# Kernel optimization log

Measured on AMD Instinct MI355X. Metric: run time of the kernel, lower is better.

## Reference

```python
import jax, jax.numpy as jnp
import numpy as np

N_NODES = 100000
N_EDGES = 3200000
IN_C, HID_C, OUT_C = 64, 64, 32


def setup_inputs() -> dict:
    key = jax.random.key(0)
    ks = jax.random.split(key, 8)
    x = jax.random.normal(ks[0], (N_NODES, IN_C), dtype=jnp.float32)
    edge_index = jax.random.randint(ks[1], (2, N_EDGES), 0, N_NODES, dtype=jnp.int64)
    s1 = 1.0 / np.sqrt(IN_C)
    s2 = 1.0 / np.sqrt(HID_C)
    W1l = jax.random.uniform(ks[2], (IN_C, HID_C), jnp.float32, -s1, s1)
    b1l = jnp.zeros((HID_C,), jnp.float32)
    W1r = jax.random.uniform(ks[3], (IN_C, HID_C), jnp.float32, -s1, s1)
    W2l = jax.random.uniform(ks[4], (HID_C, OUT_C), jnp.float32, -s2, s2)
    b2l = jnp.zeros((OUT_C,), jnp.float32)
    W2r = jax.random.uniform(ks[5], (HID_C, OUT_C), jnp.float32, -s2, s2)
    return {"x": x, "edge_index": edge_index, "W1l": W1l, "b1l": b1l,
            "W1r": W1r, "W2l": W2l, "b2l": b2l, "W2r": W2r}


def _sage_conv(x, src, dst, Wl, bl, Wr):
    # mean-aggregate source features onto destination nodes
    msg = x[src]                                              # [E, d] gather
    summed = jax.ops.segment_sum(msg, dst, num_segments=N_NODES)
    deg = jax.ops.segment_sum(jnp.ones((src.shape[0],), x.dtype), dst,
                              num_segments=N_NODES)
    agg = summed / jnp.maximum(deg, 1.0)[:, None]             # [N, d]
    return agg @ Wl + bl + x @ Wr                             # lin_l(agg)+lin_r(x)


def reference(x, edge_index, W1l, b1l, W1r, W2l, b2l, W2r):
    src, dst = edge_index[0], edge_index[1]
    h = jax.nn.relu(_sage_conv(x, src, dst, W1l, b1l, W1r))
    # dropout is identity in eval mode
    return _sage_conv(h, src, dst, W2l, b2l, W2r)
```

## Files before the change

### kernel.cpp

```cpp
#include <hip/hip_runtime.h>
#include <hip/hip_bf16.h>

#define N_NODES 100000
#define N_EDGES 3200000
#define NBKT 391
#define BKT_CAP 10240
#define NOCT (N_NODES / 8)

typedef __hip_bfloat16 bf16;
typedef unsigned int uint;
typedef __attribute__((ext_vector_type(8))) short bf16x8;
typedef __attribute__((ext_vector_type(4))) float f32x4;

__device__ __forceinline__ float b2f(bf16 v) { return __bfloat162float(v); }

__device__ __forceinline__ float bits2f(unsigned short w) {
    union { unsigned short u; bf16 b; } c;
    c.u = w;
    return __bfloat162float(c.b);
}
__device__ __forceinline__ unsigned short f2bits(float f) {
    return (unsigned short)(__float_as_uint(f) >> 16);
}
__device__ __forceinline__ unsigned short f2bf_bits(float f) {
    bf16 b = __float2bfloat16(f);
    unsigned short u;
    __builtin_memcpy(&u, &b, 2);
    return u;
}
__device__ __forceinline__ float lo16f(uint w) { return __uint_as_float(w << 16); }
__device__ __forceinline__ float hi16f(uint w) { return __uint_as_float(w & 0xffff0000u); }

__device__ __forceinline__ int get_idx(const void* ei, long long pos, int is64) {
    if (is64) return (int)((const long long*)ei)[pos];
    return ((const int*)ei)[pos];
}
__device__ __forceinline__ float get_f(const void* p, long long pos, int isbf) {
    if (isbf) return b2f(((const bf16*)p)[pos]);
    return ((const float*)p)[pos];
}

__global__ void detect_kernel(const void* __restrict__ x,
                              const void* __restrict__ ei,
                              int* __restrict__ flags) {
    int lane = threadIdx.x;
    const unsigned short* xw = (const unsigned short*)x;
    float v = bits2f(xw[2 * lane]);
    bool plaus = (v == v) && fabsf(v) > 1e-3f && fabsf(v) < 1e2f;
    unsigned long long m1 = __ballot(plaus);
    const int* iw = (const int*)ei;
    bool z = (iw[2 * lane + 1] == 0);
    unsigned long long m2 = __ballot(z);
    if (lane == 0) {
        flags[0] = (__popcll(m1) >= 32) ? 1 : 0;
        flags[1] = (__popcll(m2) == 64) ? 1 : 0;
    }
}

__global__ __launch_bounds__(256) void transpose_kernel(
    const void* __restrict__ x, uint4* __restrict__ xt,
    const int* __restrict__ flags) {
    if (!flags[0]) return;
    int i = blockIdx.x * 256 + threadIdx.x;
    if (i >= N_NODES * 4) return;
    int node = i >> 2, cz = i & 3;
    const uint4* x4 = (const uint4*)x;
    uint4 a = x4[(long long)node * 8 + cz * 2];
    uint4 b = x4[(long long)node * 8 + cz * 2 + 1];
    long long o = (long long)cz * (N_NODES * 2) + (long long)node * 2;
    xt[o] = a;
    xt[o + 1] = b;
}

__global__ __launch_bounds__(256) void scatterA_kernel(
    const void* __restrict__ ei, int* __restrict__ bucket_cursor,
    uint* __restrict__ bucket_data, const int* __restrict__ flags) {
    __shared__ int lhist[NBKT];
    __shared__ int lbase[NBKT];
    int is64 = flags[1];
    int t = threadIdx.x;
    int chunk0 = blockIdx.x * 8192;
    int dreg[32];

    for (int i = t; i < NBKT; i += 256) lhist[i] = 0;
    __syncthreads();
#pragma unroll
    for (int j = 0; j < 32; j++) {
        int e = chunk0 + j * 256 + t;
        int d = -1;
        if (e < N_EDGES) {
            d = get_idx(ei, (long long)N_EDGES + e, is64);
            atomicAdd(&lhist[d >> 8], 1);
        }
        dreg[j] = d;
    }
    __syncthreads();
    for (int i = t; i < NBKT; i += 256) {
        int c = lhist[i];
        lbase[i] = c ? atomicAdd(&bucket_cursor[i], c) : 0;
        lhist[i] = 0;
    }
    __syncthreads();
#pragma unroll
    for (int j = 0; j < 32; j++) {
        int e = chunk0 + j * 256 + t;
        int d = dreg[j];
        if (d >= 0) {
            int s = get_idx(ei, e, is64);
            int b = d >> 8;
            int o = lbase[b] + atomicAdd(&lhist[b], 1);
            if (o < BKT_CAP)
                bucket_data[(long long)b * BKT_CAP + o] = ((uint)(d & 255) << 17) | (uint)s;
        }
    }
}

__global__ void scanBuckets_kernel(const int* __restrict__ cnt,
                                   int* __restrict__ base) {
    __shared__ int buf[512];
    int t = threadIdx.x;
    int v = (t < NBKT) ? cnt[t] : 0;
    buf[t] = v;
    __syncthreads();
    for (int off = 1; off < 512; off <<= 1) {
        int add = (t >= off) ? buf[t - off] : 0;
        __syncthreads();
        buf[t] += add;
        __syncthreads();
    }
    if (t < NBKT) base[t] = buf[t] - v;
}

__global__ __launch_bounds__(256) void csrB_kernel(
    const int* __restrict__ bucket_cnt, const int* __restrict__ bucket_base,
    const uint* __restrict__ bucket_data, int* __restrict__ csr_src,
    int* __restrict__ row_start) {
    __shared__ int lh[256];
    __shared__ int buf[256];
    int b = blockIdx.x;
    int t = threadIdx.x;
    int cnt = bucket_cnt[b];
    if (cnt > BKT_CAP) cnt = BKT_CAP;
    int base = bucket_base[b];
    const uint* bd = bucket_data + (long long)b * BKT_CAP;

    lh[t] = 0;
    __syncthreads();
    for (int i = t; i < cnt; i += 256) atomicAdd(&lh[bd[i] >> 17], 1);
    __syncthreads();
    int v = lh[t];
    buf[t] = v;
    __syncthreads();
    for (int off = 1; off < 256; off <<= 1) {
        int add = (t >= off) ? buf[t - off] : 0;
        __syncthreads();
        buf[t] += add;
        __syncthreads();
    }
    int excl = buf[t] - v;
    int g = (b << 8) + t;
    if (g < N_NODES) row_start[g] = base + excl;
    lh[t] = excl;
    __syncthreads();
    for (int i = t; i < cnt; i += 256) {
        uint e = bd[i];
        int o = atomicAdd(&lh[e >> 17], 1);
        csr_src[base + o] = (int)(e & 0x1FFFFu);
    }
    if (b == 0 && t == 0) row_start[N_NODES] = N_EDGES;
}

#define ACCF4(acc, v, v2)                                                        \
    acc[0] += __uint_as_float((v).x) + __uint_as_float((v2).x);                   \
    acc[1] += __uint_as_float((v).y) + __uint_as_float((v2).y);                   \
    acc[2] += __uint_as_float((v).z) + __uint_as_float((v2).z);                   \
    acc[3] += __uint_as_float((v).w) + __uint_as_float((v2).w);

__device__ __forceinline__ void slice_gather8(
    const uint* __restrict__ su, const int* __restrict__ row_start,
    const int* __restrict__ csr_src, int nb0, int g8, int c8, int lane,
    float& a0, float& a1, int& dg_out) {
    int rl = (lane <= 8) ? row_start[nb0 + lane] : 0;
    int sg = __shfl(rl, g8 >> 3, 64);
    int eg = __shfl(rl, (g8 >> 3) + 1, 64);
    int dg = eg - sg;
    int maxd = dg;
    maxd = max(maxd, __shfl_xor(maxd, 8, 64));
    maxd = max(maxd, __shfl_xor(maxd, 16, 64));
    maxd = max(maxd, __shfl_xor(maxd, 32, 64));

    float s0f = 0.0f, s1f = 0.0f;
    for (int base = 0; base < maxd; base += 8) {
        int pf = sg + base + c8;
        int sreg = (pf < eg) ? __builtin_nontemporal_load(csr_src + pf) : 0;
        int ss[8];
#pragma unroll
        for (int u = 0; u < 8; u++) ss[u] = __shfl(sreg, g8 + u, 64);
        uint wv[8];
#pragma unroll
        for (int u = 0; u < 8; u++)
            wv[u] = (base + u < dg) ? su[(ss[u] << 3) + c8] : 0u;
#pragma unroll
        for (int u = 0; u < 8; u++) {
            s0f += lo16f(wv[u]);
            s1f += hi16f(wv[u]);
        }
    }
    a0 = s0f;
    a1 = s1f;
    dg_out = dg;
}

__global__ __launch_bounds__(256) void gather1_kernel(
    const void* __restrict__ x, const uint* __restrict__ xtu,
    const int* __restrict__ row_start, const int* __restrict__ csr_src,
    bf16* __restrict__ aggbuf, const int* __restrict__ flags, int cz_base) {
    int isbf = flags[0];
    int t = threadIdx.x;
    int lane = t & 63;
    int w = t >> 6;
    int bid = blockIdx.x;

    if (isbf) {
        int cz = cz_base + ((bid & 7) >> 2);
        int wid = ((((bid >> 3) << 2) | (bid & 3)) << 2) + w;
        int nw = gridDim.x * 2;
        int g8 = lane & 0x38, c8 = lane & 7;
        int g = lane >> 3;
        const uint* su = xtu + (long long)cz * (N_NODES * 8);
        uint* ag = (uint*)aggbuf;
        for (int oct = wid; oct < NOCT; oct += nw) {
            int nb0 = oct * 8;
            float a0, a1;
            int dg;
            slice_gather8(su, row_start, csr_src, nb0, g8, c8, lane, a0, a1, dg);
            float inv = 1.0f / fmaxf((float)dg, 1.0f);
            uint pk = (uint)f2bf_bits(a0 * inv) |
                      ((uint)f2bf_bits(a1 * inv) << 16);
            __builtin_nontemporal_store(pk, ag + (nb0 + g) * 32 + cz * 8 + c8);
        }
    } else {
        if (cz_base != 0) return;
        int gw = (bid * 256 + t) >> 6;
        int nwv = (gridDim.x * 256) >> 6;
        int e4 = lane >> 4, q16 = lane & 15;
        const uint4* xf = (const uint4*)x;
        for (int p = gw; p * 2 < N_NODES; p += nwv) {
            int na = p * 2, nb = p * 2 + 1;
            int sa = row_start[na], ea = row_start[na + 1];
            int sb = row_start[nb], eb = row_start[nb + 1];
            int da = ea - sa, db = eb - sb;
            int maxd = max(da, db);
            float accA[4] = {0, 0, 0, 0};
            float accB[4] = {0, 0, 0, 0};
            for (int off = 0; off < maxd; off += 16) {
                int iA0 = sa + off + e4, iA1 = iA0 + 4, iA2 = iA0 + 8, iA3 = iA0 + 12;
                int iB0 = sb + off + e4, iB1 = iB0 + 4, iB2 = iB0 + 8, iB3 = iB0 + 12;
                int sA0 = (iA0 < ea) ? csr_src[iA0] : -1;
                int sA1 = (iA1 < ea) ? csr_src[iA1] : -1;
                int sA2 = (iA2 < ea) ? csr_src[iA2] : -1;
                int sA3 = (iA3 < ea) ? csr_src[iA3] : -1;
                int sB0 = (iB0 < eb) ? csr_src[iB0] : -1;
                int sB1 = (iB1 < eb) ? csr_src[iB1] : -1;
                int sB2 = (iB2 < eb) ? csr_src[iB2] : -1;
                int sB3 = (iB3 < eb) ? csr_src[iB3] : -1;
                uint4 vA0 = {0,0,0,0}, vA1 = {0,0,0,0}, vA2 = {0,0,0,0}, vA3 = {0,0,0,0};
                uint4 vB0 = {0,0,0,0}, vB1 = {0,0,0,0}, vB2 = {0,0,0,0}, vB3 = {0,0,0,0};
                if (sA0 >= 0) vA0 = xf[sA0 * 16 + q16];
                if (sA1 >= 0) vA1 = xf[sA1 * 16 + q16];
                if (sA2 >= 0) vA2 = xf[sA2 * 16 + q16];
                if (sA3 >= 0) vA3 = xf[sA3 * 16 + q16];
                if (sB0 >= 0) vB0 = xf[sB0 * 16 + q16];
                if (sB1 >= 0) vB1 = xf[sB1 * 16 + q16];
                if (sB2 >= 0) vB2 = xf[sB2 * 16 + q16];
                if (sB3 >= 0) vB3 = xf[sB3 * 16 + q16];
                ACCF4(accA, vA0, vA1)
                ACCF4(accA, vA2, vA3)
                ACCF4(accB, vB0, vB1)
                ACCF4(accB, vB2, vB3)
            }
#pragma unroll
            for (int m = 16; m <= 32; m <<= 1)
#pragma unroll
                for (int k = 0; k < 4; k++) {
                    accA[k] += __shfl_xor(accA[k], m, 64);
                    accB[k] += __shfl_xor(accB[k], m, 64);
                }
            float avA = 0.0f, avB = 0.0f;
#pragma unroll
            for (int k = 0; k < 4; k++) {
                float vA = __shfl(accA[k], lane >> 2, 64);
                float vB = __shfl(accB[k], lane >> 2, 64);
                avA = ((lane & 3) == k) ? vA : avA;
                avB = ((lane & 3) == k) ? vB : avB;
            }
            avA *= 1.0f / fmaxf((float)da, 1.0f);
            avB *= 1.0f / fmaxf((float)db, 1.0f);
            aggbuf[(long long)na * 64 + lane] = __float2bfloat16(avA);
            aggbuf[(long long)nb * 64 + lane] = __float2bfloat16(avB);
        }
    }
}

__global__ __launch_bounds__(256) void gemm1_kernel(
    const void* __restrict__ x, const bf16* __restrict__ aggbuf,
    const void* __restrict__ W1l, const void* __restrict__ b1l,
    const void* __restrict__ W1r, const void* __restrict__ W2l,
    const void* __restrict__ b2l, const void* __restrict__ W2r,
    bf16* __restrict__ zbufT, bf16* __restrict__ rbufT,
    const int* __restrict__ flags) {
    __shared__ __align__(16) unsigned short sW1t[64][136];
    __shared__ __align__(16) unsigned short sA[64][136];
    __shared__ __align__(16) unsigned short sW2t[64][72];
    __shared__ __align__(16) unsigned short sH[64][72];
    __shared__ float sB1[64];
    __shared__ float sB2[32];

    int isbf = flags[0];
    int t = threadIdx.x;
    int n0 = blockIdx.x * 64;

    for (int i = t; i < 64 * 128; i += 256) {
        int n = i & 63, k = i >> 6;
        unsigned short v;
        if (isbf)
            v = (k < 64) ? ((const unsigned short*)W1l)[k * 64 + n]
                         : ((const unsigned short*)W1r)[(k - 64) * 64 + n];
        else
            v = f2bits((k < 64) ? ((const float*)W1l)[k * 64 + n]
                                : ((const float*)W1r)[(k - 64) * 64 + n]);
        sW1t[n][k] = v;
    }
    for (int i = t; i < 64 * 64; i += 256) {
        int n = i & 63, k = i >> 6;
        unsigned short v;
        if (isbf)
            v = (n < 32) ? ((const unsigned short*)W2l)[k * 32 + n]
                         : ((const unsigned short*)W2r)[k * 32 + (n - 32)];
        else
            v = f2bits((n < 32) ? ((const float*)W2l)[k * 32 + n]
                                : ((const float*)W2r)[k * 32 + (n - 32)]);
        sW2t[n][k] = v;
    }
    if (t < 64) sB1[t] = get_f(b1l, t, isbf);
    if (t < 32) sB2[t] = get_f(b2l, t, isbf);

    const uint4* ag4 = (const uint4*)aggbuf;
    if (isbf) {
        const uint4* x4 = (const uint4*)x;
        for (int i = t; i < 64 * 16; i += 256) {
            int m = i >> 4, c = i & 15;
            int nn = min(n0 + m, N_NODES - 1);
            uint4 v = (c < 8) ? ag4[(long long)nn * 8 + c]
                              : x4[(long long)nn * 8 + (c - 8)];
            *(uint4*)&sA[m][c * 8] = v;
        }
    } else {
        for (int i = t; i < 64 * 8; i += 256) {
            int m = i >> 3, c = i & 7;
            int nn = min(n0 + m, N_NODES - 1);
            *(uint4*)&sA[m][c * 8] = ag4[(long long)nn * 8 + c];
        }
        const float* xf = (const float*)x;
        for (int i = t; i < 64 * 64; i += 256) {
            int m = i >> 6, c = i & 63;
            int nn = min(n0 + m, N_NODES - 1);
            sA[m][64 + c] = f2bf_bits(xf[(long long)nn * 64 + c]);
        }
    }
    __syncthreads();

    int w = t >> 6, lane = t & 63;
    int mbase = w * 16;
    int q = lane >> 4, r15 = lane & 15;
    f32x4 acc1[4] = {{0,0,0,0},{0,0,0,0},{0,0,0,0},{0,0,0,0}};
#pragma unroll
    for (int ks = 0; ks < 4; ks++) {
        bf16x8 afrag = *(const bf16x8*)&sA[mbase + r15][ks * 32 + q * 8];
#pragma unroll
        for (int nt = 0; nt < 4; nt++) {
            bf16x8 bfrag = *(const bf16x8*)&sW1t[nt * 16 + r15][ks * 32 + q * 8];
            acc1[nt] = __builtin_amdgcn_mfma_f32_16x16x32_bf16(afrag, bfrag, acc1[nt], 0, 0, 0);
        }
    }
#pragma unroll
    for (int nt = 0; nt < 4; nt++) {
        int col = nt * 16 + r15;
        float bias = sB1[col];
#pragma unroll
        for (int rr = 0; rr < 4; rr++) {
            int m = mbase + q * 4 + rr;
            sH[m][col] = f2bf_bits(fmaxf(acc1[nt][rr] + bias, 0.0f));
        }
    }
    __syncthreads();

    f32x4 acc2[4] = {{0,0,0,0},{0,0,0,0},{0,0,0,0},{0,0,0,0}};
#pragma unroll
    for (int ks = 0; ks < 2; ks++) {
        bf16x8 afrag = *(const bf16x8*)&sH[mbase + r15][ks * 32 + q * 8];
#pragma unroll
        for (int nt = 0; nt < 4; nt++) {
            bf16x8 bfrag = *(const bf16x8*)&sW2t[nt * 16 + r15][ks * 32 + q * 8];
            acc2[nt] = __builtin_amdgcn_mfma_f32_16x16x32_bf16(afrag, bfrag, acc2[nt], 0, 0, 0);
        }
    }
#pragma unroll
    for (int nt = 0; nt < 4; nt++) {
        int col = nt * 16 + r15;
#pragma unroll
        for (int rr = 0; rr < 4; rr++) {
            int m = mbase + q * 4 + rr;
            int n = n0 + m;
            if (n < N_NODES) {
                float v = acc2[nt][rr];
                if (col < 32) {
                    zbufT[(long long)(col >> 4) * (N_NODES * 16) +
                          (long long)n * 16 + (col & 15)] = __float2bfloat16(v);
                } else {
                    int c2 = col - 32;
                    rbufT[(long long)(c2 >> 4) * (N_NODES * 16) +
                          (long long)n * 16 + (c2 & 15)] =
                        __float2bfloat16(v + sB2[c2]);
                }
            }
        }
    }
}

__global__ __launch_bounds__(256) void node2_kernel(
    const int* __restrict__ row_start, const int* __restrict__ csr_src,
    const uint* __restrict__ zTu, const bf16* __restrict__ rbufT,
    void* __restrict__ out, const int* __restrict__ flags) {
    int isbf = flags[0];
    int t = threadIdx.x;
    int lane = t & 63;
    int w = t >> 6;
    int bid = blockIdx.x;
    int cz = (bid & 7) >> 2;
    int wid = ((((bid >> 3) << 2) | (bid & 3)) << 2) + w;
    int nw = gridDim.x * 2;
    int g8 = lane & 0x38, c8 = lane & 7;
    int g = lane >> 3;
    const uint* su = zTu + (long long)cz * (N_NODES * 8);
    const uint* ru = (const uint*)(rbufT + (long long)cz * (N_NODES * 16));

    for (int oct = wid; oct < NOCT; oct += nw) {
        int nb0 = oct * 8;
        float a0, a1;
        int dg;
        slice_gather8(su, row_start, csr_src, nb0, g8, c8, lane, a0, a1, dg);
        float inv = 1.0f / fmaxf((float)dg, 1.0f);
        int n = nb0 + g;
        uint rb = __builtin_nontemporal_load(ru + n * 8 + c8);
        float r0 = a0 * inv + lo16f(rb);
        float r1 = a1 * inv + hi16f(rb);
        if (isbf) {
            uint pk = (uint)f2bf_bits(r0) | ((uint)f2bf_bits(r1) << 16);
            __builtin_nontemporal_store(pk, (uint*)out + n * 16 + cz * 8 + c8);
        } else {
            float* of = (float*)out;
            __builtin_nontemporal_store(r0, of + (long long)n * 32 + cz * 16 + 2 * c8);
            __builtin_nontemporal_store(r1, of + (long long)n * 32 + cz * 16 + 2 * c8 + 1);
        }
    }
}

extern "C" void kernel_launch(void* const* d_in, const int* in_sizes, int n_in,
                              void* d_out, int out_size, void* d_ws, size_t ws_size,
                              hipStream_t stream) {
    const void* x = d_in[0];
    const void* ei = d_in[1];
    const void* W1l = d_in[2];
    const void* b1l = d_in[3];
    const void* W1r = d_in[4];
    const void* W2l = d_in[5];
    const void* b2l = d_in[6];
    const void* W2r = d_in[7];

    char* ws = (char*)d_ws;
    uint* bucket_data = (uint*)ws;
    bf16* aggbuf = (bf16*)ws;
    int* csr_src = (int*)(ws + 16015424);
    int* row_start = (int*)(ws + 28815424);
    int* bucket_cursor = (int*)(ws + 29215488);
    int* bucket_base = (int*)(ws + 29217088);
    uint* xtu = (uint*)(ws + 29218688);
    bf16* zbufT = (bf16*)(ws + 29218688);
    bf16* rbufT = (bf16*)(ws + 35618688);
    int* flags = (int*)(ws + 42018688);

    hipMemsetAsync(bucket_cursor, 0, NBKT * 4, stream);

    detect_kernel<<<1, 64, 0, stream>>>(x, ei, flags);
    transpose_kernel<<<1563, 256, 0, stream>>>(x, (uint4*)xtu, flags);
    scatterA_kernel<<<NBKT, 256, 0, stream>>>(ei, bucket_cursor, bucket_data, flags);
    scanBuckets_kernel<<<1, 512, 0, stream>>>(bucket_cursor, bucket_base);
    csrB_kernel<<<NBKT, 256, 0, stream>>>(bucket_cursor, bucket_base, bucket_data,
                                          csr_src, row_start);
    gather1_kernel<<<4096, 256, 0, stream>>>(x, xtu, row_start, csr_src, aggbuf,
                                             flags, 0);
    gather1_kernel<<<4096, 256, 0, stream>>>(x, xtu, row_start, csr_src, aggbuf,
                                             flags, 2);
    gemm1_kernel<<<1563, 256, 0, stream>>>(x, aggbuf, W1l, b1l, W1r, W2l, b2l,
                                           W2r, zbufT, rbufT, flags);
    node2_kernel<<<4096, 256, 0, stream>>>(row_start, csr_src, (const uint*)zbufT,
                                           rbufT, d_out, flags);
}
```

Before: 381.5 us.

## Replace layer-1 CSR gather with per-bucket LDS-accumulated gather over source-sorted edges

csrB now also writes a second copy of each bucket's packed edges, sorted by source-node group (src>>12) within the destination bucket. A new gatherT kernel gives one block per 256-destination bucket, accumulates bf16 source rows into a 64KB float LDS tile with LDS atomics, then normalises by degree and writes aggbuf. This removes the transposed-x pre-pass and the two sliced gather passes, and aims for better L2 locality on source rows. In exchange it launches only 391 heavy-LDS blocks, performs many LDS atomics, and adds an extra edge-array write in csrB.

New measurement: 380.9 us. No clear change (-0.2%).

```diff
diff --git a/kernel.cpp b/kernel.cpp
--- a/kernel.cpp
+++ b/kernel.cpp
@@ -57,21 +57,6 @@
     }
 }
 
-__global__ __launch_bounds__(256) void transpose_kernel(
-    const void* __restrict__ x, uint4* __restrict__ xt,
-    const int* __restrict__ flags) {
-    if (!flags[0]) return;
-    int i = blockIdx.x * 256 + threadIdx.x;
-    if (i >= N_NODES * 4) return;
-    int node = i >> 2, cz = i & 3;
-    const uint4* x4 = (const uint4*)x;
-    uint4 a = x4[(long long)node * 8 + cz * 2];
-    uint4 b = x4[(long long)node * 8 + cz * 2 + 1];
-    long long o = (long long)cz * (N_NODES * 2) + (long long)node * 2;
-    xt[o] = a;
-    xt[o + 1] = b;
-}
-
 __global__ __launch_bounds__(256) void scatterA_kernel(
     const void* __restrict__ ei, int* __restrict__ bucket_cursor,
     uint* __restrict__ bucket_data, const int* __restrict__ flags) {
@@ -134,9 +119,11 @@
 __global__ __launch_bounds__(256) void csrB_kernel(
     const int* __restrict__ bucket_cnt, const int* __restrict__ bucket_base,
     const uint* __restrict__ bucket_data, int* __restrict__ csr_src,
-    int* __restrict__ row_start) {
+    int* __restrict__ row_start, uint* __restrict__ tiled) {
     __shared__ int lh[256];
     __shared__ int buf[256];
+    __shared__ int gcnt[32];
+    __shared__ int gbase[32];
     int b = blockIdx.x;
     int t = threadIdx.x;
     int cnt = bucket_cnt[b];
@@ -145,8 +132,13 @@
     const uint* bd = bucket_data + (long long)b * BKT_CAP;
 
     lh[t] = 0;
-    __syncthreads();
-    for (int i = t; i < cnt; i += 256) atomicAdd(&lh[bd[i] >> 17], 1);
+    if (t < 32) gcnt[t] = 0;
+    __syncthreads();
+    for (int i = t; i < cnt; i += 256) {
+        uint e = bd[i];
+        atomicAdd(&lh[e >> 17], 1);
+        atomicAdd(&gcnt[(e & 0x1FFFFu) >> 12], 1);
+    }
     __syncthreads();
     int v = lh[t];
     buf[t] = v;
@@ -161,11 +153,20 @@
     int g = (b << 8) + t;
     if (g < N_NODES) row_start[g] = base + excl;
     lh[t] = excl;
+    if (t == 0) {
+        int run = 0;
+#pragma unroll
+        for (int k = 0; k < 32; k++) { gbase[k] = run; run += gcnt[k]; }
+    }
+    __syncthreads();
+    if (t < 32) gcnt[t] = gbase[t];
     __syncthreads();
     for (int i = t; i < cnt; i += 256) {
         uint e = bd[i];
         int o = atomicAdd(&lh[e >> 17], 1);
         csr_src[base + o] = (int)(e & 0x1FFFFu);
+        int o2 = atomicAdd(&gcnt[(e & 0x1FFFFu) >> 12], 1);
+        tiled[base + o2] = e;
     }
     if (b == 0 && t == 0) row_start[N_NODES] = N_EDGES;
 }
@@ -176,129 +177,140 @@
     acc[2] += __uint_as_float((v).z) + __uint_as_float((v2).z);                   \
     acc[3] += __uint_as_float((v).w) + __uint_as_float((v2).w);
 
-__device__ __forceinline__ void slice_gather8(
-    const uint* __restrict__ su, const int* __restrict__ row_start,
-    const int* __restrict__ csr_src, int nb0, int g8, int c8, int lane,
-    float& a0, float& a1, int& dg_out) {
-    int rl = (lane <= 8) ? row_start[nb0 + lane] : 0;
-    int sg = __shfl(rl, g8 >> 3, 64);
-    int eg = __shfl(rl, (g8 >> 3) + 1, 64);
-    int dg = eg - sg;
-    int maxd = dg;
-    maxd = max(maxd, __shfl_xor(maxd, 8, 64));
-    maxd = max(maxd, __shfl_xor(maxd, 16, 64));
-    maxd = max(maxd, __shfl_xor(maxd, 32, 64));
-
-    float s0f = 0.0f, s1f = 0.0f;
-    for (int base = 0; base < maxd; base += 8) {
-        int pf = sg + base + c8;
-        int sreg = (pf < eg) ? __builtin_nontemporal_load(csr_src + pf) : 0;
-        int ss[8];
-#pragma unroll
-        for (int u = 0; u < 8; u++) ss[u] = __shfl(sreg, g8 + u, 64);
-        uint wv[8];
-#pragma unroll
-        for (int u = 0; u < 8; u++)
-            wv[u] = (base + u < dg) ? su[(ss[u] << 3) + c8] : 0u;
-#pragma unroll
-        for (int u = 0; u < 8; u++) {
-            s0f += lo16f(wv[u]);
-            s1f += hi16f(wv[u]);
-        }
-    }
-    a0 = s0f;
-    a1 = s1f;
-    dg_out = dg;
-}
-
-__global__ __launch_bounds__(256) void gather1_kernel(
-    const void* __restrict__ x, const uint* __restrict__ xtu,
-    const int* __restrict__ row_start, const int* __restrict__ csr_src,
-    bf16* __restrict__ aggbuf, const int* __restrict__ flags, int cz_base) {
-    int isbf = flags[0];
+#define ACCADD(dl, v) {                                                          \
+    float* ap = &acc[(dl) * 64 + c8v * 8];                                       \
+    atomicAdd(ap + 0, lo16f((v).x)); atomicAdd(ap + 1, hi16f((v).x));            \
+    atomicAdd(ap + 2, lo16f((v).y)); atomicAdd(ap + 3, hi16f((v).y));            \
+    atomicAdd(ap + 4, lo16f((v).z)); atomicAdd(ap + 5, hi16f((v).z));            \
+    atomicAdd(ap + 6, lo16f((v).w)); atomicAdd(ap + 7, hi16f((v).w)); }
+
+__global__ __launch_bounds__(256) void gatherT_kernel(
+    const void* __restrict__ x, const uint* __restrict__ tiled,
+    const int* __restrict__ bucket_base, const int* __restrict__ row_start,
+    bf16* __restrict__ aggbuf, const int* __restrict__ flags) {
+    if (!flags[0]) return;
+    __shared__ float acc[256 * 64];
+    int b = blockIdx.x, t = threadIdx.x;
+    for (int i = t; i < 256 * 64; i += 256) acc[i] = 0.0f;
+    int base = bucket_base[b];
+    int cnt = ((b == NBKT - 1) ? N_EDGES : bucket_base[b + 1]) - base;
+    if (cnt > BKT_CAP) cnt = BKT_CAP;
+    const uint* seg = tiled + base;
+    const uint4* x4 = (const uint4*)x;
+    int g = t >> 3, c8v = t & 7;
+    __syncthreads();
+
+    int nFull = cnt >> 7;
+    for (int j = 0; j < nFull; j++) {
+        int e0 = (j << 7) + (g << 2);
+        uint ea = seg[e0], eb = seg[e0 + 1], ec = seg[e0 + 2], ed = seg[e0 + 3];
+        uint4 va = x4[(ea & 0x1FFFFu) * 8 + c8v];
+        uint4 vb = x4[(eb & 0x1FFFFu) * 8 + c8v];
+        uint4 vc = x4[(ec & 0x1FFFFu) * 8 + c8v];
+        uint4 vd = x4[(ed & 0x1FFFFu) * 8 + c8v];
+        ACCADD(ea >> 17, va)
+        ACCADD(eb >> 17, vb)
+        ACCADD(ec >> 17, vc)
+        ACCADD(ed >> 17, vd)
+    }
+    {
+        int tb = nFull << 7;
+#pragma unroll
+        for (int u = 0; u < 4; u++) {
+            int idx = tb + (g << 2) + u;
+            if (idx < cnt) {
+                uint e = seg[idx];
+                uint4 vv = x4[(e & 0x1FFFFu) * 8 + c8v];
+                ACCADD(e >> 17, vv)
+            }
+        }
+    }
+    __syncthreads();
+
+    uint* ag = (uint*)aggbuf;
+#pragma unroll
+    for (int it = 0; it < 8; it++) {
+        int task = it * 256 + t;
+        int node = task >> 3, q = task & 7;
+        int n = (b << 8) + node;
+        if (n < N_NODES) {
+            int deg = row_start[n + 1] - row_start[n];
+            float inv = 1.0f / fmaxf((float)deg, 1.0f);
+            float* a = &acc[node * 64 + q * 8];
+            uint4 pk;
+            pk.x = (uint)f2bf_bits(a[0] * inv) | ((uint)f2bf_bits(a[1] * inv) << 16);
+            pk.y = (uint)f2bf_bits(a[2] * inv) | ((uint)f2bf_bits(a[3] * inv) << 16);
+            pk.z = (uint)f2bf_bits(a[4] * inv) | ((uint)f2bf_bits(a[5] * inv) << 16);
+            pk.w = (uint)f2bf_bits(a[6] * inv) | ((uint)f2bf_bits(a[7] * inv) << 16);
+            *(uint4*)(ag + (long long)n * 32 + q * 4) = pk;
+        }
+    }
+}
+
+__global__ __launch_bounds__(256) void gather1_fp32_kernel(
+    const void* __restrict__ x, const int* __restrict__ row_start,
+    const int* __restrict__ csr_src, bf16* __restrict__ aggbuf,
+    const int* __restrict__ flags) {
+    if (flags[0]) return;
     int t = threadIdx.x;
     int lane = t & 63;
-    int w = t >> 6;
-    int bid = blockIdx.x;
-
-    if (isbf) {
-        int cz = cz_base + ((bid & 7) >> 2);
-        int wid = ((((bid >> 3) << 2) | (bid & 3)) << 2) + w;
-        int nw = gridDim.x * 2;
-        int g8 = lane & 0x38, c8 = lane & 7;
-        int g = lane >> 3;
-        const uint* su = xtu + (long long)cz * (N_NODES * 8);
-        uint* ag = (uint*)aggbuf;
-        for (int oct = wid; oct < NOCT; oct += nw) {
-            int nb0 = oct * 8;
-            float a0, a1;
-            int dg;
-            slice_gather8(su, row_start, csr_src, nb0, g8, c8, lane, a0, a1, dg);
-            float inv = 1.0f / fmaxf((float)dg, 1.0f);
-            uint pk = (uint)f2bf_bits(a0 * inv) |
-                      ((uint)f2bf_bits(a1 * inv) << 16);
-            __builtin_nontemporal_store(pk, ag + (nb0 + g) * 32 + cz * 8 + c8);
-        }
-    } else {
-        if (cz_base != 0) return;
-        int gw = (bid * 256 + t) >> 6;
-        int nwv = (gridDim.x * 256) >> 6;
-        int e4 = lane >> 4, q16 = lane & 15;
-        const uint4* xf = (const uint4*)x;
-        for (int p = gw; p * 2 < N_NODES; p += nwv) {
-            int na = p * 2, nb = p * 2 + 1;
-            int sa = row_start[na], ea = row_start[na + 1];
-            int sb = row_start[nb], eb = row_start[nb + 1];
-            int da = ea - sa, db = eb - sb;
-            int maxd = max(da, db);
-            float accA[4] = {0, 0, 0, 0};
-            float accB[4] = {0, 0, 0, 0};
-            for (int off = 0; off < maxd; off += 16) {
-                int iA0 = sa + off + e4, iA1 = iA0 + 4, iA2 = iA0 + 8, iA3 = iA0 + 12;
-                int iB0 = sb + off + e4, iB1 = iB0 + 4, iB2 = iB0 + 8, iB3 = iB0 + 12;
-                int sA0 = (iA0 < ea) ? csr_src[iA0] : -1;
-                int sA1 = (iA1 < ea) ? csr_src[iA1] : -1;
-                int sA2 = (iA2 < ea) ? csr_src[iA2] : -1;
-                int sA3 = (iA3 < ea) ? csr_src[iA3] : -1;
-                int sB0 = (iB0 < eb) ? csr_src[iB0] : -1;
-                int sB1 = (iB1 < eb) ? csr_src[iB1] : -1;
-                int sB2 = (iB2 < eb) ? csr_src[iB2] : -1;
-                int sB3 = (iB3 < eb) ? csr_src[iB3] : -1;
-                uint4 vA0 = {0,0,0,0}, vA1 = {0,0,0,0}, vA2 = {0,0,0,0}, vA3 = {0,0,0,0};
-                uint4 vB0 = {0,0,0,0}, vB1 = {0,0,0,0}, vB2 = {0,0,0,0}, vB3 = {0,0,0,0};
-                if (sA0 >= 0) vA0 = xf[sA0 * 16 + q16];
-                if (sA1 >= 0) vA1 = xf[sA1 * 16 + q16];
-                if (sA2 >= 0) vA2 = xf[sA2 * 16 + q16];
-                if (sA3 >= 0) vA3 = xf[sA3 * 16 + q16];
-                if (sB0 >= 0) vB0 = xf[sB0 * 16 + q16];
-                if (sB1 >= 0) vB1 = xf[sB1 * 16 + q16];
-                if (sB2 >= 0) vB2 = xf[sB2 * 16 + q16];
-                if (sB3 >= 0) vB3 = xf[sB3 * 16 + q16];
-                ACCF4(accA, vA0, vA1)
-                ACCF4(accA, vA2, vA3)
-                ACCF4(accB, vB0, vB1)
-                ACCF4(accB, vB2, vB3)
+    int gw = (blockIdx.x * 256 + t) >> 6;
+    int nwv = (gridDim.x * 256) >> 6;
+    int e4 = lane >> 4, q16 = lane & 15;
+    const uint4* xf = (const uint4*)x;
+    for (int p = gw; p * 2 < N_NODES; p += nwv) {
+        int na = p * 2, nb = p * 2 + 1;
+        int sa = row_start[na], ea = row_start[na + 1];
+        int sb = row_start[nb], eb = row_start[nb + 1];
+        int da = ea - sa, db = eb - sb;
+        int maxd = max(da, db);
+        float accA[4] = {0, 0, 0, 0};
+        float accB[4] = {0, 0, 0, 0};
+        for (int off = 0; off < maxd; off += 16) {
+            int iA0 = sa + off + e4, iA1 = iA0 + 4, iA2 = iA0 + 8, iA3 = iA0 + 12;
+            int iB0 = sb + off + e4, iB1 = iB0 + 4, iB2 = iB0 + 8, iB3 = iB0 + 12;
+            int sA0 = (iA0 < ea) ? csr_src[iA0] : -1;
+            int sA1 = (iA1 < ea) ? csr_src[iA1] : -1;
+            int sA2 = (iA2 < ea) ? csr_src[iA2] : -1;
+            int sA3 = (iA3 < ea) ? csr_src[iA3] : -1;
+            int sB0 = (iB0 < eb) ? csr_src[iB0] : -1;
+            int sB1 = (iB1 < eb) ? csr_src[iB1] : -1;
+            int sB2 = (iB2 < eb) ? csr_src[iB2] : -1;
+            int sB3 = (iB3 < eb) ? csr_src[iB3] : -1;
+            uint4 vA0 = {0,0,0,0}, vA1 = {0,0,0,0}, vA2 = {0,0,0,0}, vA3 = {0,0,0,0};
+            uint4 vB0 = {0,0,0,0}, vB1 = {0,0,0,0}, vB2 = {0,0,0,0}, vB3 = {0,0,0,0};
+            if (sA0 >= 0) vA0 = xf[sA0 * 16 + q16];
+            if (sA1 >= 0) vA1 = xf[sA1 * 16 + q16];
+            if (sA2 >= 0) vA2 = xf[sA2 * 16 + q16];
+            if (sA3 >= 0) vA3 = xf[sA3 * 16 + q16];
+            if (sB0 >= 0) vB0 = xf[sB0 * 16 + q16];
+            if (sB1 >= 0) vB1 = xf[sB1 * 16 + q16];
+            if (sB2 >= 0) vB2 = xf[sB2 * 16 + q16];
+            if (sB3 >= 0) vB3 = xf[sB3 * 16 + q16];
+            ACCF4(accA, vA0, vA1)
+            ACCF4(accA, vA2, vA3)
+            ACCF4(accB, vB0, vB1)
+            ACCF4(accB, vB2, vB3)
+        }
+#pragma unroll
+        for (int m = 16; m <= 32; m <<= 1)
+#pragma unroll
+            for (int k = 0; k < 4; k++) {
+                accA[k] += __shfl_xor(accA[k], m, 64);
+                accB[k] += __shfl_xor(accB[k], m, 64);
             }
-#pragma unroll
-            for (int m = 16; m <= 32; m <<= 1)
-#pragma unroll
-                for (int k = 0; k < 4; k++) {
-                    accA[k] += __shfl_xor(accA[k], m, 64);
-                    accB[k] += __shfl_xor(accB[k], m, 64);
-                }
-            float avA = 0.0f, avB = 0.0f;
-#pragma unroll
-            for (int k = 0; k < 4; k++) {
-                float vA = __shfl(accA[k], lane >> 2, 64);
-                float vB = __shfl(accB[k], lane >> 2, 64);
-                avA = ((lane & 3) == k) ? vA : avA;
-                avB = ((lane & 3) == k) ? vB : avB;
-            }
-            avA *= 1.0f / fmaxf((float)da, 1.0f);
-            avB *= 1.0f / fmaxf((float)db, 1.0f);
-            aggbuf[(long long)na * 64 + lane] = __float2bfloat16(avA);
-            aggbuf[(long long)nb * 64 + lane] = __float2bfloat16(avB);
-        }
+        float avA = 0.0f, avB = 0.0f;
+#pragma unroll
+        for (int k = 0; k < 4; k++) {
+            float vA = __shfl(accA[k], lane >> 2, 64);
+            float vB = __shfl(accB[k], lane >> 2, 64);
+            avA = ((lane & 3) == k) ? vA : avA;
+            avB = ((lane & 3) == k) ? vB : avB;
+        }
+        avA *= 1.0f / fmaxf((float)da, 1.0f);
+        avB *= 1.0f / fmaxf((float)db, 1.0f);
+        aggbuf[(long long)na * 64 + lane] = __float2bfloat16(avA);
+        aggbuf[(long long)nb * 64 + lane] = __float2bfloat16(avB);
     }
 }
 
@@ -426,6 +438,41 @@
             }
         }
     }
+}
+
+__device__ __forceinline__ void slice_gather8(
+    const uint* __restrict__ su, const int* __restrict__ row_start,
+    const int* __restrict__ csr_src, int nb0, int g8, int c8, int lane,
+    float& a0, float& a1, int& dg_out) {
+    int rl = (lane <= 8) ? row_start[nb0 + lane] : 0;
+    int sg = __shfl(rl, g8 >> 3, 64);
+    int eg = __shfl(rl, (g8 >> 3) + 1, 64);
+    int dg = eg - sg;
+    int maxd = dg;
+    maxd = max(maxd, __shfl_xor(maxd, 8, 64));
+    maxd = max(maxd, __shfl_xor(maxd, 16, 64));
+    maxd = max(maxd, __shfl_xor(maxd, 32, 64));
+
+    float s0f = 0.0f, s1f = 0.0f;
+    for (int base = 0; base < maxd; base += 8) {
+        int pf = sg + base + c8;
+        int sreg = (pf < eg) ? __builtin_nontemporal_load(csr_src + pf) : 0;
+        int ss[8];
+#pragma unroll
+        for (int u = 0; u < 8; u++) ss[u] = __shfl(sreg, g8 + u, 64);
+        uint wv[8];
+#pragma unroll
+        for (int u = 0; u < 8; u++)
+            wv[u] = (base + u < dg) ? su[(ss[u] << 3) + c8] : 0u;
+#pragma unroll
+        for (int u = 0; u < 8; u++) {
+            s0f += lo16f(wv[u]);
+            s1f += hi16f(wv[u]);
+        }
+    }
+    a0 = s0f;
+    a1 = s1f;
+    dg_out = dg;
 }
 
 __global__ __launch_bounds__(256) void node2_kernel(
@@ -485,7 +532,7 @@
     int* row_start = (int*)(ws + 28815424);
     int* bucket_cursor = (int*)(ws + 29215488);
     int* bucket_base = (int*)(ws + 29217088);
-    uint* xtu = (uint*)(ws + 29218688);
+    uint* tiled_edges = (uint*)(ws + 29218688);
     bf16* zbufT = (bf16*)(ws + 29218688);
     bf16* rbufT = (bf16*)(ws + 35618688);
     int* flags = (int*)(ws + 42018688);
@@ -493,15 +540,14 @@
     hipMemsetAsync(bucket_cursor, 0, NBKT * 4, stream);
 
     detect_kernel<<<1, 64, 0, stream>>>(x, ei, flags);
-    transpose_kernel<<<1563, 256, 0, stream>>>(x, (uint4*)xtu, flags);
     scatterA_kernel<<<NBKT, 256, 0, stream>>>(ei, bucket_cursor, bucket_data, flags);
     scanBuckets_kernel<<<1, 512, 0, stream>>>(bucket_cursor, bucket_base);
     csrB_kernel<<<NBKT, 256, 0, stream>>>(bucket_cursor, bucket_base, bucket_data,
-                                          csr_src, row_start);
-    gather1_kernel<<<4096, 256, 0, stream>>>(x, xtu, row_start, csr_src, aggbuf,
-                                             flags, 0);
-    gather1_kernel<<<4096, 256, 0, stream>>>(x, xtu, row_start, csr_src, aggbuf,
-                                             flags, 2);
+                                          csr_src, row_start, tiled_edges);
+    gatherT_kernel<<<NBKT, 256, 0, stream>>>(x, tiled_edges, bucket_base,
+                                             row_start, aggbuf, flags);
+    gather1_fp32_kernel<<<3125, 256, 0, stream>>>(x, row_start, csr_src, aggbuf,
+                                                  flags);
     gemm1_kernel<<<1563, 256, 0, stream>>>(x, aggbuf, W1l, b1l, W1r, W2l, b2l,
                                            W2r, zbufT, rbufT, flags);
     node2_kernel<<<4096, 256, 0, stream>>>(row_start, csr_src, (const uint*)zbufT,
```
